# Kernel tuning notes

Measured on AMD Instinct MI355X. Metric: run time of the kernel, lower is better.

## Reference

```python
import jax, jax.numpy as jnp
import numpy as np

K_SIZE = 5  # kernel_size


def _patches(f, k):
    # f: (b, c, h, w) -> (b, c, k*k, h, w), matching torch.nn.Unfold ordering
    # (patch positions row-major (kh, kw) per channel), padding = k//2, stride 1.
    p = k // 2
    b, c, h, w = f.shape
    fp = jnp.pad(f, ((0, 0), (0, 0), (p, p), (p, p)))
    slices = [fp[:, :, i:i + h, j:j + w] for i in range(k) for j in range(k)]
    return jnp.stack(slices, axis=2)


def _conv1x1(w, b, f):
    # w: (out, in), b: (out,), f: (b, in, h, w)
    return jnp.einsum('oc,bchw->bohw', w, f) + b[None, :, None, None]


def setup_inputs() -> dict:
    key = jax.random.key(0)
    ks = jax.random.split(key, 8)
    B, XC, YC, FT, H, W = 4, 64, 64, 64, 128, 128
    x = jax.random.normal(ks[0], (B, XC, H, W), dtype=jnp.float32)
    y = jax.random.normal(ks[1], (B, YC, H, W), dtype=jnp.float32)
    sx = 1.0 / np.sqrt(XC)
    sy = 1.0 / np.sqrt(YC)
    sf = 1.0 / np.sqrt(FT)
    wx = jax.random.uniform(ks[2], (FT, XC), jnp.float32, -sx, sx)
    bx = jax.random.uniform(ks[3], (FT,), jnp.float32, -sx, sx)
    wy = jax.random.uniform(ks[4], (FT, YC), jnp.float32, -sy, sy)
    by = jax.random.uniform(ks[5], (FT,), jnp.float32, -sy, sy)
    wo = jax.random.uniform(ks[6], (XC, FT), jnp.float32, -sf, sf)
    bo = jax.random.uniform(ks[7], (XC,), jnp.float32, -sf, sf)
    return {"x": x, "y": y, "wx": wx, "bx": bx, "wy": wy, "by": by, "wo": wo, "bo": bo}


def reference(x, y, wx, bx, wy, by, wo, bo):
    k = K_SIZE
    q = _conv1x1(wy, by, y)            # (b, feat, h, w): Q (the q axis of size 1 is squeezed)
    Kp = _patches(q, k)                # (b, feat, k^2, h, w): unfold(conv_y(y))
    v = _conv1x1(wx, bx, x)            # (b, feat, h, w)
    Vp = _patches(v, k)                # (b, feat, k^2, h, w): unfold(conv_x(x))
    A = jnp.einsum('bckhw,bchw->bkhw', Kp, q)   # scores over k^2 neighbors
    A = jax.nn.softmax(A, axis=1)               # softmax over dim=1 (k^2)
    out = jnp.einsum('bkhw,bckhw->bchw', A, Vp)  # aggregate values
    out = _conv1x1(wo, bo, out)
    return out + x
```

## Files before the change

### kernel.cpp

```cpp
#include <hip/hip_runtime.h>

#define HH   128
#define WW   128
#define HW   (HH * WW)
#define CC   64
#define TILE 8
#define HALO 12
#define NHP  (HALO * HALO)

typedef unsigned int uint32;
typedef _Float16 h2   __attribute__((ext_vector_type(2)));
typedef __fp16   h2b  __attribute__((ext_vector_type(2)));
typedef _Float16 h8   __attribute__((ext_vector_type(8)));
typedef float    f32x4 __attribute__((ext_vector_type(4)));

__device__ __forceinline__ uint32 pkrtz(float a, float b) {
    h2b r = __builtin_amdgcn_cvt_pkrtz(a, b);
    return __builtin_bit_cast(uint32, r);
}
__device__ __forceinline__ float dot2(uint32 a, uint32 b, float c) {
#if __has_builtin(__builtin_amdgcn_fdot2)
    return __builtin_amdgcn_fdot2(__builtin_bit_cast(h2b, a),
                                  __builtin_bit_cast(h2b, b), c, false);
#else
    h2 x = __builtin_bit_cast(h2, a), y = __builtin_bit_cast(h2, b);
    return c + (float)x.x * (float)y.x + (float)x.y * (float)y.y;
#endif
}
__device__ __forceinline__ f32x4 mfma16(uint4 a, uint4 b, f32x4 c) {
    return __builtin_amdgcn_mfma_f32_16x16x32_f16(
        __builtin_bit_cast(h8, a), __builtin_bit_cast(h8, b), c, 0, 0, 0);
}
__device__ __forceinline__ uint4 pack_w8(const float* __restrict__ w) {
    const float4 lo = *(const float4*)w;
    const float4 hi = *(const float4*)(w + 4);
    uint4 r;
    r.x = pkrtz(lo.x, lo.y); r.y = pkrtz(lo.z, lo.w);
    r.z = pkrtz(hi.x, hi.y); r.w = pkrtz(hi.z, hi.w);
    return r;
}

__global__ __launch_bounds__(256, 4)
void fused_attn(const float* __restrict__ x, const float* __restrict__ y,
                const float* __restrict__ wx, const float* __restrict__ bx,
                const float* __restrict__ wy, const float* __restrict__ by,
                const float* __restrict__ wo, const float* __restrict__ bo,
                float* __restrict__ out)
{
    __shared__ uint32 Ah[NHP * 32];
    __shared__ uint32 Bh[NHP * 32];

    const int lin  = blockIdx.x;
    const int xcd  = lin & 7;
    const int rr   = lin >> 3;
    const int b    = xcd >> 1;
    const int half = xcd & 1;
    const int ty0  = (((rr >> 4) + half * 8)) * TILE;
    const int tx0  = (rr & 15) * TILE;

    const int t = threadIdx.x;

    for (int i = t; i < NHP * 8; i += 256) {
        const int c   = i / NHP;
        const int pix = i - c * NHP;
        const int hy  = pix / HALO, hx = pix - hy * HALO;
        int gy = ty0 + hy - 2, gx = tx0 + hx - 2;
        const bool ok = ((unsigned)gy < HH) & ((unsigned)gx < WW);
        if (!ok) { gy = 0; gx = 0; }
        const size_t base = (size_t)b * CC * HW + (size_t)(c * 8) * HW
                          + (size_t)gy * WW + gx;
        float yv[8], xv[8];
        #pragma unroll
        for (int j = 0; j < 8; ++j) {
            yv[j] = y[base + (size_t)j * HW];
            xv[j] = x[base + (size_t)j * HW];
        }
        uint4 yq, xq;
        yq.x = pkrtz(yv[0], yv[1]); yq.y = pkrtz(yv[2], yv[3]);
        yq.z = pkrtz(yv[4], yv[5]); yq.w = pkrtz(yv[6], yv[7]);
        xq.x = pkrtz(xv[0], xv[1]); xq.y = pkrtz(xv[2], xv[3]);
        xq.z = pkrtz(xv[4], xv[5]); xq.w = pkrtz(xv[6], xv[7]);
        const int w0 = (c ^ (pix & 7)) * 4;
        *(uint4*)&Ah[pix * 32 + w0] = yq;
        *(uint4*)&Bh[pix * 32 + w0] = xq;
    }
    __syncthreads();

    const int wv = t >> 6;
    const int ln = t & 63;
    const int lm = ln & 15;
    const int qd = ln >> 4;

    f32x4 accq[9], accv[9];
    uint2 xres[4];
    {
        const uint4 aq0 = pack_w8(wy + (wv * 16 + lm) * CC + qd * 8);
        const uint4 aq1 = pack_w8(wy + (wv * 16 + lm) * CC + qd * 8 + 32);
        const uint4 av0 = pack_w8(wx + (wv * 16 + lm) * CC + qd * 8);
        const uint4 av1 = pack_w8(wx + (wv * 16 + lm) * CC + qd * 8 + 32);
        #pragma unroll
        for (int nt = 0; nt < 9; ++nt) {
            const int px = nt * 16 + lm, sw = px & 7;
            const uint4 b0 = *(const uint4*)&Ah[px * 32 + ((qd    ) ^ sw) * 4];
            const uint4 b1 = *(const uint4*)&Ah[px * 32 + ((qd + 4) ^ sw) * 4];
            f32x4 a = {0.f, 0.f, 0.f, 0.f};
            a = mfma16(aq0, b0, a); a = mfma16(aq1, b1, a); accq[nt] = a;
            const uint4 c0 = *(const uint4*)&Bh[px * 32 + ((qd    ) ^ sw) * 4];
            const uint4 c1 = *(const uint4*)&Bh[px * 32 + ((qd + 4) ^ sw) * 4];
            f32x4 v = {0.f, 0.f, 0.f, 0.f};
            v = mfma16(av0, c0, v); v = mfma16(av1, c1, v); accv[nt] = v;
        }
        #pragma unroll
        for (int nt = 0; nt < 4; ++nt) {
            const int px = nt * 16 + lm;
            const int hpix = ((px >> 3) + 2) * HALO + (px & 7) + 2;
            const int chunk = wv * 2 + (qd >> 1);
            xres[nt] = *(const uint2*)
                &Bh[hpix * 32 + (chunk ^ (hpix & 7)) * 4 + (qd & 1) * 2];
        }
    }
    __syncthreads();

    {
        const float4 bq = *(const float4*)(by + wv * 16 + qd * 4);
        const float4 bv = *(const float4*)(bx + wv * 16 + qd * 4);
        const int chunk = wv * 2 + (qd >> 1);
        #pragma unroll
        for (int nt = 0; nt < 9; ++nt) {
            const int px = nt * 16 + lm;
            const int hy = px / HALO, hx = px - hy * HALO;
            const int gy = ty0 + hy - 2, gx = tx0 + hx - 2;
            uint2 wq = {0u, 0u}, wvv = {0u, 0u};
            if (((unsigned)gy < HH) & ((unsigned)gx < WW)) {
                wq.x  = pkrtz(accq[nt].x + bq.x, accq[nt].y + bq.y);
                wq.y  = pkrtz(accq[nt].z + bq.z, accq[nt].w + bq.w);
                wvv.x = pkrtz(accv[nt].x + bv.x, accv[nt].y + bv.y);
                wvv.y = pkrtz(accv[nt].z + bv.z, accv[nt].w + bv.w);
            }
            const int off = px * 32 + (chunk ^ (px & 7)) * 4 + (qd & 1) * 2;
            *(uint2*)&Ah[off] = wq;
            *(uint2*)&Bh[off] = wvv;
        }
    }
    __syncthreads();

    const int p    = t >> 2, sub = t & 3;
    const int py   = p >> 3, px8 = p & 7;
    const int crow = (py + 2) * HALO + (px8 + 2);

    uint32 qc[8];
    {
        const int c0 = ((2 * sub) ^ (crow & 7)) * 4;
        const int c1 = ((2 * sub + 1) ^ (crow & 7)) * 4;
        *(uint4*)&qc[0] = *(const uint4*)&Ah[crow * 32 + c0];
        *(uint4*)&qc[4] = *(const uint4*)&Ah[crow * 32 + c1];
    }

    float sc[25];
    #pragma unroll
    for (int dy = 0; dy < 5; ++dy)
        #pragma unroll
        for (int dx = 0; dx < 5; ++dx) {
            const int nrow = (py + dy) * HALO + (px8 + dx);
            const int c0 = ((2 * sub) ^ (nrow & 7)) * 4;
            const int c1 = ((2 * sub + 1) ^ (nrow & 7)) * 4;
            const uint4 r0 = *(const uint4*)&Ah[nrow * 32 + c0];
            const uint4 r1 = *(const uint4*)&Ah[nrow * 32 + c1];
            float s = 0.f;
            s = dot2(qc[0], r0.x, s); s = dot2(qc[1], r0.y, s);
            s = dot2(qc[2], r0.z, s); s = dot2(qc[3], r0.w, s);
            s = dot2(qc[4], r1.x, s); s = dot2(qc[5], r1.y, s);
            s = dot2(qc[6], r1.z, s); s = dot2(qc[7], r1.w, s);
            s += __shfl_xor(s, 1);
            s += __shfl_xor(s, 2);
            sc[dy * 5 + dx] = s;
        }

    float mx = sc[0];
    #pragma unroll
    for (int k = 1; k < 25; ++k) mx = fmaxf(mx, sc[k]);
    float sum = 0.f;
    #pragma unroll
    for (int k = 0; k < 25; ++k) { sc[k] = __expf(sc[k] - mx); sum += sc[k]; }
    const float inv = 1.f / sum;

    h2 ag[8];
    #pragma unroll
    for (int k = 0; k < 8; ++k) ag[k] = (h2)(_Float16)0;
    #pragma unroll
    for (int dy = 0; dy < 5; ++dy)
        #pragma unroll
        for (int dx = 0; dx < 5; ++dx) {
            const int nrow = (py + dy) * HALO + (px8 + dx);
            const int c0 = ((2 * sub) ^ (nrow & 7)) * 4;
            const int c1 = ((2 * sub + 1) ^ (nrow & 7)) * 4;
            const uint4 r0 = *(const uint4*)&Bh[nrow * 32 + c0];
            const uint4 r1 = *(const uint4*)&Bh[nrow * 32 + c1];
            const _Float16 af = (_Float16)(sc[dy * 5 + dx] * inv);
            const h2 a2 = {af, af};
            ag[0] += a2 * __builtin_bit_cast(h2, r0.x);
            ag[1] += a2 * __builtin_bit_cast(h2, r0.y);
            ag[2] += a2 * __builtin_bit_cast(h2, r0.z);
            ag[3] += a2 * __builtin_bit_cast(h2, r0.w);
            ag[4] += a2 * __builtin_bit_cast(h2, r1.x);
            ag[5] += a2 * __builtin_bit_cast(h2, r1.y);
            ag[6] += a2 * __builtin_bit_cast(h2, r1.z);
            ag[7] += a2 * __builtin_bit_cast(h2, r1.w);
        }

    __syncthreads();
    {
        const int c0 = ((2 * sub) ^ (p & 7)) * 4;
        const int c1 = ((2 * sub + 1) ^ (p & 7)) * 4;
        uint4 w0, w1;
        w0.x = __builtin_bit_cast(uint32, ag[0]); w0.y = __builtin_bit_cast(uint32, ag[1]);
        w0.z = __builtin_bit_cast(uint32, ag[2]); w0.w = __builtin_bit_cast(uint32, ag[3]);
        w1.x = __builtin_bit_cast(uint32, ag[4]); w1.y = __builtin_bit_cast(uint32, ag[5]);
        w1.z = __builtin_bit_cast(uint32, ag[6]); w1.w = __builtin_bit_cast(uint32, ag[7]);
        *(uint4*)&Ah[p * 32 + c0] = w0;
        *(uint4*)&Ah[p * 32 + c1] = w1;
    }
    __syncthreads();

    {
        const uint4 a0 = pack_w8(wo + (wv * 16 + lm) * CC + qd * 8);
        const uint4 a1 = pack_w8(wo + (wv * 16 + lm) * CC + qd * 8 + 32);
        const float4 bq = *(const float4*)(bo + wv * 16 + qd * 4);
        #pragma unroll
        for (int nt = 0; nt < 4; ++nt) {
            const int px = nt * 16 + lm, sw = px & 7;
            const uint4 b0 = *(const uint4*)&Ah[px * 32 + ((qd    ) ^ sw) * 4];
            const uint4 b1 = *(const uint4*)&Ah[px * 32 + ((qd + 4) ^ sw) * 4];
            f32x4 a = {0.f, 0.f, 0.f, 0.f};
            a = mfma16(a0, b0, a);
            a = mfma16(a1, b1, a);
            const int gh = ty0 + (px >> 3), gw = tx0 + (px & 7);
            const h2 xp0 = __builtin_bit_cast(h2, xres[nt].x);
            const h2 xp1 = __builtin_bit_cast(h2, xres[nt].y);
            const float rv[4] = {(float)xp0.x, (float)xp0.y,
                                 (float)xp1.x, (float)xp1.y};
            const float av4[4] = {a.x + bq.x, a.y + bq.y, a.z + bq.z, a.w + bq.w};
            #pragma unroll
            for (int r = 0; r < 4; ++r) {
                const int oc = wv * 16 + qd * 4 + r;
                const size_t ad = (size_t)(b * CC + oc) * HW + (size_t)gh * WW + gw;
                out[ad] = av4[r] + rv[r];
            }
        }
    }
}

extern "C" void kernel_launch(void* const* d_in, const int* in_sizes, int n_in,
                              void* d_out, int out_size, void* d_ws, size_t ws_size,
                              hipStream_t stream) {
    const float* x  = (const float*)d_in[0];
    const float* y  = (const float*)d_in[1];
    const float* wx = (const float*)d_in[2];
    const float* bx = (const float*)d_in[3];
    const float* wy = (const float*)d_in[4];
    const float* by = (const float*)d_in[5];
    const float* wo = (const float*)d_in[6];
    const float* bo = (const float*)d_in[7];
    float* out = (float*)d_out;
    (void)d_ws; (void)ws_size;

    fused_attn<<<dim3(1024), 256, 0, stream>>>(x, y, wx, bx, wy, by, wo, bo, out);
}
```

Baseline: 116.2 us.

## Enlarge spatial tile to 16x16 with 1024-thread blocks to cut halo overhead

Raises the per-block output tile from 8x8 to 16x16, with a 20x20 halo and 1024 threads per block, so the block count drops from 1024 to 256. This cuts redundant halo loads and 1x1 conv recompute: the halo-to-tile ratio falls from 144/64 to 400/256. The input loads become float2 pairs, the LDS swizzle becomes (row>>1)&7, and the MFMA work for the projection and output conv is redistributed across 16 waves. The trade-off is larger LDS per block, with LDS, launch bounds and 1024-thread blocks together limiting occupancy to one block per CU. With only 256 blocks the grid may also underfill the GPU's CUs.

```diff
diff --git a/kernel.cpp b/kernel.cpp
--- a/kernel.cpp
+++ b/kernel.cpp
@@ -4,9 +4,10 @@
 #define WW   128
 #define HW   (HH * WW)
 #define CC   64
-#define TILE 8
-#define HALO 12
+#define TILE 16
+#define HALO 20
 #define NHP  (HALO * HALO)
+#define SWZ(r) (((r) >> 1) & 7)
 
 typedef unsigned int uint32;
 typedef _Float16 h2   __attribute__((ext_vector_type(2)));
@@ -40,7 +41,7 @@
     return r;
 }
 
-__global__ __launch_bounds__(256, 4)
+__global__ __launch_bounds__(1024, 4)
 void fused_attn(const float* __restrict__ x, const float* __restrict__ y,
                 const float* __restrict__ wx, const float* __restrict__ bx,
                 const float* __restrict__ wy, const float* __restrict__ by,
@@ -55,34 +56,41 @@
     const int rr   = lin >> 3;
     const int b    = xcd >> 1;
     const int half = xcd & 1;
-    const int ty0  = (((rr >> 4) + half * 8)) * TILE;
-    const int tx0  = (rr & 15) * TILE;
+    const int ty0  = ((rr >> 3) + half * 4) * TILE;
+    const int tx0  = (rr & 7) * TILE;
 
     const int t = threadIdx.x;
 
-    for (int i = t; i < NHP * 8; i += 256) {
-        const int c   = i / NHP;
-        const int pix = i - c * NHP;
-        const int hy  = pix / HALO, hx = pix - hy * HALO;
+    for (int i = t; i < NHP * 8 / 2; i += 1024) {
+        const int c   = i / 200;
+        const int rem = i - c * 200;
+        const int hy  = rem / 10;
+        const int hx  = (rem - hy * 10) * 2;
+        const int pix = hy * HALO + hx;
         int gy = ty0 + hy - 2, gx = tx0 + hx - 2;
-        const bool ok = ((unsigned)gy < HH) & ((unsigned)gx < WW);
+        const bool ok = ((unsigned)gy < HH) & ((unsigned)gx < (WW - 1));
         if (!ok) { gy = 0; gx = 0; }
         const size_t base = (size_t)b * CC * HW + (size_t)(c * 8) * HW
                           + (size_t)gy * WW + gx;
-        float yv[8], xv[8];
+        float2 yv[8], xv[8];
         #pragma unroll
         for (int j = 0; j < 8; ++j) {
-            yv[j] = y[base + (size_t)j * HW];
-            xv[j] = x[base + (size_t)j * HW];
-        }
-        uint4 yq, xq;
-        yq.x = pkrtz(yv[0], yv[1]); yq.y = pkrtz(yv[2], yv[3]);
-        yq.z = pkrtz(yv[4], yv[5]); yq.w = pkrtz(yv[6], yv[7]);
-        xq.x = pkrtz(xv[0], xv[1]); xq.y = pkrtz(xv[2], xv[3]);
-        xq.z = pkrtz(xv[4], xv[5]); xq.w = pkrtz(xv[6], xv[7]);
-        const int w0 = (c ^ (pix & 7)) * 4;
-        *(uint4*)&Ah[pix * 32 + w0] = yq;
-        *(uint4*)&Bh[pix * 32 + w0] = xq;
+            yv[j] = *(const float2*)(y + base + (size_t)j * HW);
+            xv[j] = *(const float2*)(x + base + (size_t)j * HW);
+        }
+        uint4 q0, q1;
+        q0.x = pkrtz(yv[0].x, yv[1].x); q0.y = pkrtz(yv[2].x, yv[3].x);
+        q0.z = pkrtz(yv[4].x, yv[5].x); q0.w = pkrtz(yv[6].x, yv[7].x);
+        q1.x = pkrtz(yv[0].y, yv[1].y); q1.y = pkrtz(yv[2].y, yv[3].y);
+        q1.z = pkrtz(yv[4].y, yv[5].y); q1.w = pkrtz(yv[6].y, yv[7].y);
+        *(uint4*)&Ah[pix * 32 + (c ^ SWZ(pix)) * 4]           = q0;
+        *(uint4*)&Ah[(pix + 1) * 32 + (c ^ SWZ(pix + 1)) * 4] = q1;
+        q0.x = pkrtz(xv[0].x, xv[1].x); q0.y = pkrtz(xv[2].x, xv[3].x);
+        q0.z = pkrtz(xv[4].x, xv[5].x); q0.w = pkrtz(xv[6].x, xv[7].x);
+        q1.x = pkrtz(xv[0].y, xv[1].y); q1.y = pkrtz(xv[2].y, xv[3].y);
+        q1.z = pkrtz(xv[4].y, xv[5].y); q1.w = pkrtz(xv[6].y, xv[7].y);
+        *(uint4*)&Bh[pix * 32 + (c ^ SWZ(pix)) * 4]           = q0;
+        *(uint4*)&Bh[(pix + 1) * 32 + (c ^ SWZ(pix + 1)) * 4] = q1;
     }
     __syncthreads();
 
@@ -90,68 +98,75 @@
     const int ln = t & 63;
     const int lm = ln & 15;
     const int qd = ln >> 4;
-
-    f32x4 accq[9], accv[9];
+    const int ot = wv & 3;
+
+    f32x4 accq[7], accv[7];
     uint2 xres[4];
     {
-        const uint4 aq0 = pack_w8(wy + (wv * 16 + lm) * CC + qd * 8);
-        const uint4 aq1 = pack_w8(wy + (wv * 16 + lm) * CC + qd * 8 + 32);
-        const uint4 av0 = pack_w8(wx + (wv * 16 + lm) * CC + qd * 8);
-        const uint4 av1 = pack_w8(wx + (wv * 16 + lm) * CC + qd * 8 + 32);
-        #pragma unroll
-        for (int nt = 0; nt < 9; ++nt) {
-            const int px = nt * 16 + lm, sw = px & 7;
-            const uint4 b0 = *(const uint4*)&Ah[px * 32 + ((qd    ) ^ sw) * 4];
-            const uint4 b1 = *(const uint4*)&Ah[px * 32 + ((qd + 4) ^ sw) * 4];
-            f32x4 a = {0.f, 0.f, 0.f, 0.f};
-            a = mfma16(aq0, b0, a); a = mfma16(aq1, b1, a); accq[nt] = a;
-            const uint4 c0 = *(const uint4*)&Bh[px * 32 + ((qd    ) ^ sw) * 4];
-            const uint4 c1 = *(const uint4*)&Bh[px * 32 + ((qd + 4) ^ sw) * 4];
-            f32x4 v = {0.f, 0.f, 0.f, 0.f};
-            v = mfma16(av0, c0, v); v = mfma16(av1, c1, v); accv[nt] = v;
-        }
-        #pragma unroll
-        for (int nt = 0; nt < 4; ++nt) {
-            const int px = nt * 16 + lm;
-            const int hpix = ((px >> 3) + 2) * HALO + (px & 7) + 2;
-            const int chunk = wv * 2 + (qd >> 1);
-            xres[nt] = *(const uint2*)
-                &Bh[hpix * 32 + (chunk ^ (hpix & 7)) * 4 + (qd & 1) * 2];
-        }
-    }
-    __syncthreads();
-
-    {
-        const float4 bq = *(const float4*)(by + wv * 16 + qd * 4);
-        const float4 bv = *(const float4*)(bx + wv * 16 + qd * 4);
-        const int chunk = wv * 2 + (qd >> 1);
-        #pragma unroll
-        for (int nt = 0; nt < 9; ++nt) {
-            const int px = nt * 16 + lm;
-            const int hy = px / HALO, hx = px - hy * HALO;
-            const int gy = ty0 + hy - 2, gx = tx0 + hx - 2;
-            uint2 wq = {0u, 0u}, wvv = {0u, 0u};
-            if (((unsigned)gy < HH) & ((unsigned)gx < WW)) {
-                wq.x  = pkrtz(accq[nt].x + bq.x, accq[nt].y + bq.y);
-                wq.y  = pkrtz(accq[nt].z + bq.z, accq[nt].w + bq.w);
-                wvv.x = pkrtz(accv[nt].x + bv.x, accv[nt].y + bv.y);
-                wvv.y = pkrtz(accv[nt].z + bv.z, accv[nt].w + bv.w);
+        const uint4 aq0 = pack_w8(wy + (ot * 16 + lm) * CC + qd * 8);
+        const uint4 aq1 = pack_w8(wy + (ot * 16 + lm) * CC + qd * 8 + 32);
+        const uint4 av0 = pack_w8(wx + (ot * 16 + lm) * CC + qd * 8);
+        const uint4 av1 = pack_w8(wx + (ot * 16 + lm) * CC + qd * 8 + 32);
+        #pragma unroll
+        for (int k = 0; k < 7; ++k) {
+            const int j = wv + k * 16;
+            if (j < 100) {
+                const int px = (j >> 2) * 16 + lm, sw = SWZ(px);
+                const uint4 b0 = *(const uint4*)&Ah[px * 32 + ((qd    ) ^ sw) * 4];
+                const uint4 b1 = *(const uint4*)&Ah[px * 32 + ((qd + 4) ^ sw) * 4];
+                f32x4 a = {0.f, 0.f, 0.f, 0.f};
+                a = mfma16(aq0, b0, a); a = mfma16(aq1, b1, a); accq[k] = a;
+                const uint4 c0 = *(const uint4*)&Bh[px * 32 + ((qd    ) ^ sw) * 4];
+                const uint4 c1 = *(const uint4*)&Bh[px * 32 + ((qd + 4) ^ sw) * 4];
+                f32x4 v = {0.f, 0.f, 0.f, 0.f};
+                v = mfma16(av0, c0, v); v = mfma16(av1, c1, v); accv[k] = v;
             }
-            const int off = px * 32 + (chunk ^ (px & 7)) * 4 + (qd & 1) * 2;
-            *(uint2*)&Ah[off] = wq;
-            *(uint2*)&Bh[off] = wvv;
+        }
+        #pragma unroll
+        for (int k = 0; k < 4; ++k) {
+            const int px = ((wv >> 2) + k * 4) * 16 + lm;
+            const int hpix = ((px >> 4) + 2) * HALO + (px & 15) + 2;
+            const int chunk = ot * 2 + (qd >> 1);
+            xres[k] = *(const uint2*)
+                &Bh[hpix * 32 + (chunk ^ SWZ(hpix)) * 4 + (qd & 1) * 2];
+        }
+    }
+    __syncthreads();
+
+    {
+        const float4 bq = *(const float4*)(by + ot * 16 + qd * 4);
+        const float4 bv = *(const float4*)(bx + ot * 16 + qd * 4);
+        const int chunk = ot * 2 + (qd >> 1);
+        #pragma unroll
+        for (int k = 0; k < 7; ++k) {
+            const int j = wv + k * 16;
+            if (j < 100) {
+                const int px = (j >> 2) * 16 + lm;
+                const int hy = px / HALO, hx = px - hy * HALO;
+                const int gy = ty0 + hy - 2, gx = tx0 + hx - 2;
+                uint2 wq = {0u, 0u}, wvv = {0u, 0u};
+                if (((unsigned)gy < HH) & ((unsigned)gx < WW)) {
+                    wq.x  = pkrtz(accq[k].x + bq.x, accq[k].y + bq.y);
+                    wq.y  = pkrtz(accq[k].z + bq.z, accq[k].w + bq.w);
+                    wvv.x = pkrtz(accv[k].x + bv.x, accv[k].y + bv.y);
+                    wvv.y = pkrtz(accv[k].z + bv.z, accv[k].w + bv.w);
+                }
+                const int off = px * 32 + (chunk ^ SWZ(px)) * 4 + (qd & 1) * 2;
+                *(uint2*)&Ah[off] = wq;
+                *(uint2*)&Bh[off] = wvv;
+            }
         }
     }
     __syncthreads();
 
     const int p    = t >> 2, sub = t & 3;
-    const int py   = p >> 3, px8 = p & 7;
-    const int crow = (py + 2) * HALO + (px8 + 2);
+    const int py   = p >> 4, pxl = p & 15;
+    const int crow = (py + 2) * HALO + (pxl + 2);
 
     uint32 qc[8];
     {
-        const int c0 = ((2 * sub) ^ (crow & 7)) * 4;
-        const int c1 = ((2 * sub + 1) ^ (crow & 7)) * 4;
+        const int c0 = ((2 * sub)     ^ SWZ(crow)) * 4;
+        const int c1 = ((2 * sub + 1) ^ SWZ(crow)) * 4;
         *(uint4*)&qc[0] = *(const uint4*)&Ah[crow * 32 + c0];
         *(uint4*)&qc[4] = *(const uint4*)&Ah[crow * 32 + c1];
     }
@@ -161,9 +176,9 @@
     for (int dy = 0; dy < 5; ++dy)
         #pragma unroll
         for (int dx = 0; dx < 5; ++dx) {
-            const int nrow = (py + dy) * HALO + (px8 + dx);
-            const int c0 = ((2 * sub) ^ (nrow & 7)) * 4;
-            const int c1 = ((2 * sub + 1) ^ (nrow & 7)) * 4;
+            const int nrow = (py + dy) * HALO + (pxl + dx);
+            const int c0 = ((2 * sub)     ^ SWZ(nrow)) * 4;
+            const int c1 = ((2 * sub + 1) ^ SWZ(nrow)) * 4;
             const uint4 r0 = *(const uint4*)&Ah[nrow * 32 + c0];
             const uint4 r1 = *(const uint4*)&Ah[nrow * 32 + c1];
             float s = 0.f;
@@ -191,9 +206,9 @@
     for (int dy = 0; dy < 5; ++dy)
         #pragma unroll
         for (int dx = 0; dx < 5; ++dx) {
-            const int nrow = (py + dy) * HALO + (px8 + dx);
-            const int c0 = ((2 * sub) ^ (nrow & 7)) * 4;
-            const int c1 = ((2 * sub + 1) ^ (nrow & 7)) * 4;
+            const int nrow = (py + dy) * HALO + (pxl + dx);
+            const int c0 = ((2 * sub)     ^ SWZ(nrow)) * 4;
+            const int c1 = ((2 * sub + 1) ^ SWZ(nrow)) * 4;
             const uint4 r0 = *(const uint4*)&Bh[nrow * 32 + c0];
             const uint4 r1 = *(const uint4*)&Bh[nrow * 32 + c1];
             const _Float16 af = (_Float16)(sc[dy * 5 + dx] * inv);
@@ -210,8 +225,8 @@
 
     __syncthreads();
     {
-        const int c0 = ((2 * sub) ^ (p & 7)) * 4;
-        const int c1 = ((2 * sub + 1) ^ (p & 7)) * 4;
+        const int c0 = ((2 * sub)     ^ SWZ(p)) * 4;
+        const int c1 = ((2 * sub + 1) ^ SWZ(p)) * 4;
         uint4 w0, w1;
         w0.x = __builtin_bit_cast(uint32, ag[0]); w0.y = __builtin_bit_cast(uint32, ag[1]);
         w0.z = __builtin_bit_cast(uint32, ag[2]); w0.w = __builtin_bit_cast(uint32, ag[3]);
@@ -223,26 +238,26 @@
     __syncthreads();
 
     {
-        const uint4 a0 = pack_w8(wo + (wv * 16 + lm) * CC + qd * 8);
-        const uint4 a1 = pack_w8(wo + (wv * 16 + lm) * CC + qd * 8 + 32);
-        const float4 bq = *(const float4*)(bo + wv * 16 + qd * 4);
-        #pragma unroll
-        for (int nt = 0; nt < 4; ++nt) {
-            const int px = nt * 16 + lm, sw = px & 7;
+        const uint4 a0 = pack_w8(wo + (ot * 16 + lm) * CC + qd * 8);
+        const uint4 a1 = pack_w8(wo + (ot * 16 + lm) * CC + qd * 8 + 32);
+        const float4 bq = *(const float4*)(bo + ot * 16 + qd * 4);
+        #pragma unroll
+        for (int k = 0; k < 4; ++k) {
+            const int px = ((wv >> 2) + k * 4) * 16 + lm, sw = SWZ(px);
             const uint4 b0 = *(const uint4*)&Ah[px * 32 + ((qd    ) ^ sw) * 4];
             const uint4 b1 = *(const uint4*)&Ah[px * 32 + ((qd + 4) ^ sw) * 4];
             f32x4 a = {0.f, 0.f, 0.f, 0.f};
             a = mfma16(a0, b0, a);
             a = mfma16(a1, b1, a);
-            const int gh = ty0 + (px >> 3), gw = tx0 + (px & 7);
-            const h2 xp0 = __builtin_bit_cast(h2, xres[nt].x);
-            const h2 xp1 = __builtin_bit_cast(h2, xres[nt].y);
+            const int gh = ty0 + (px >> 4), gw = tx0 + (px & 15);
+            const h2 xp0 = __builtin_bit_cast(h2, xres[k].x);
+            const h2 xp1 = __builtin_bit_cast(h2, xres[k].y);
             const float rv[4] = {(float)xp0.x, (float)xp0.y,
                                  (float)xp1.x, (float)xp1.y};
             const float av4[4] = {a.x + bq.x, a.y + bq.y, a.z + bq.z, a.w + bq.w};
             #pragma unroll
             for (int r = 0; r < 4; ++r) {
-                const int oc = wv * 16 + qd * 4 + r;
+                const int oc = ot * 16 + qd * 4 + r;
                 const size_t ad = (size_t)(b * CC + oc) * HW + (size_t)gh * WW + gw;
                 out[ad] = av4[r] + rv[r];
             }
@@ -264,5 +279,5 @@
     float* out = (float*)d_out;
     (void)d_ws; (void)ws_size;
 
-    fused_attn<<<dim3(1024), 256, 0, stream>>>(x, y, wx, bx, wy, by, wo, bo, out);
-}
+    fused_attn<<<dim3(256), 1024, 0, stream>>>(x, y, wx, bx, wy, by, wo, bo, out);
+}
```

Result: no change. 114.5 us (-1.5%).
